# Optimization experiments

Hardware: AMD Instinct MI355X
Metric: run time of the kernel (lower is better)

## Reference

```python
import jax, jax.numpy as jnp
import numpy as np

N = 50000       # num_entities / nodes
E = 100000      # edges
K = 8           # incoming edge-graph neighbors per edge
D_NODE = 64
D_EDGE = 64
H = 4
DH = D_EDGE // H
DIN = D_EDGE + 2 * D_NODE  # [edge_feat, node_feat[src], node_feat[dst]]


def setup_inputs() -> dict:
    key = jax.random.key(0)
    ks = jax.random.split(key, 6)
    node_features = jax.random.normal(ks[0], (N, D_NODE), jnp.float32)
    edge_features = jax.random.normal(ks[1], (E, D_EDGE), jnp.float32)
    edge_index = jax.random.randint(ks[2], (2, E), 0, N)
    node_tiers = jax.random.randint(ks[3], (N,), 0, 4, dtype=jnp.int32)
    # edge adjacency (line graph): each edge attends to K other edges
    adj_dst = jnp.repeat(jnp.arange(E), K)                       # [A]
    adj_src = jax.random.randint(ks[4], (E * K,), 0, E)          # [A]
    # learned params: two EdgeAttention layers, each Wq/Wk/Wv [DIN,D_EDGE], Wo [D_EDGE,D_EDGE]
    wkeys = jax.random.split(ks[5], 8)
    def w(k, fan_in, fan_out):
        return jax.random.normal(k, (fan_in, fan_out), jnp.float32) * np.float32(1.0 / np.sqrt(fan_in))
    params = {}
    for li in (1, 2):
        base = (li - 1) * 4
        params[f'l{li}_Wq'] = w(wkeys[base + 0], DIN, D_EDGE)
        params[f'l{li}_Wk'] = w(wkeys[base + 1], DIN, D_EDGE)
        params[f'l{li}_Wv'] = w(wkeys[base + 2], DIN, D_EDGE)
        params[f'l{li}_Wo'] = w(wkeys[base + 3], D_EDGE, D_EDGE)
    return dict(node_features=node_features, edge_features=edge_features,
                edge_index=edge_index, node_tiers=node_tiers,
                adj_src=adj_src, adj_dst=adj_dst, **params)


def _edge_attention(node_f, edge_f, edge_index, adj_src, adj_dst, Wq, Wk, Wv, Wo):
    # x: edge feature conditioned on endpoint node features  [E, DIN]
    x = jnp.concatenate([edge_f, node_f[edge_index[0]], node_f[edge_index[1]]], axis=-1)
    q = (x @ Wq).reshape(E, H, DH)
    k = (x @ Wk).reshape(E, H, DH)
    v = (x @ Wv).reshape(E, H, DH)
    scale = np.float32(1.0 / np.sqrt(DH))
    # scores per adjacency pair  [A, H]
    s = jnp.einsum('ahd,ahd->ah', q[adj_dst], k[adj_src]) * scale
    # segment softmax over incoming neighbors of each dst edge
    m = jax.ops.segment_max(s, adj_dst, num_segments=E)          # [E, H]
    e = jnp.exp(s - m[adj_dst])                                   # [A, H]
    denom = jax.ops.segment_sum(e, adj_dst, num_segments=E)      # [E, H]
    alpha = e / denom[adj_dst]                                    # [A, H]
    out = jax.ops.segment_sum(alpha[..., None] * v[adj_src], adj_dst, num_segments=E)  # [E,H,DH]
    return edge_f + out.reshape(E, D_EDGE) @ Wo                   # residual


def reference(node_features, edge_features, edge_index, node_tiers, adj_src, adj_dst,
              l1_Wq, l1_Wk, l1_Wv, l1_Wo, l2_Wq, l2_Wk, l2_Wv, l2_Wo):
    ef = _edge_attention(node_features, edge_features, edge_index, adj_src, adj_dst,
                         l1_Wq, l1_Wk, l1_Wv, l1_Wo)
    ef = _edge_attention(node_features, ef, edge_index, adj_src, adj_dst,
                         l2_Wq, l2_Wk, l2_Wv, l2_Wo)
    return ef  # updated edge features of the output DeltaGraph
```

## Files before the change

kernel.cpp:

```cpp
#include <hip/hip_runtime.h>

#define NE 100000
#define NN 50000

typedef short short8 __attribute__((ext_vector_type(8)));
typedef float f32x4 __attribute__((ext_vector_type(4)));
typedef unsigned short ushort;

__device__ inline ushort f2bf(float f) {
    unsigned int u = __float_as_uint(f);
    u += 0x7FFFu + ((u >> 16) & 1u);
    return (ushort)(u >> 16);
}
__device__ inline float bf2f(ushort u) {
    return __uint_as_float((unsigned int)u << 16);
}

__device__ inline short8 pack_bf8(float4 a, float4 b) {
    short8 r;
    r[0] = (short)f2bf(a.x); r[1] = (short)f2bf(a.y);
    r[2] = (short)f2bf(a.z); r[3] = (short)f2bf(a.w);
    r[4] = (short)f2bf(b.x); r[5] = (short)f2bf(b.y);
    r[6] = (short)f2bf(b.z); r[7] = (short)f2bf(b.w);
    return r;
}

__global__ __launch_bounds__(256) void prep_qkv_w(
    const float* __restrict__ Wq, const float* __restrict__ Wk,
    const float* __restrict__ Wv, ushort* __restrict__ wf)
{
    int idx = blockIdx.x * 256 + threadIdx.x;
    if (idx >= 6 * 12 * 64) return;
    int lane = idx & 63;
    int st = idx >> 6;
    int s = st / 12, t = st % 12;
    int n = t * 16 + (lane & 15);
    int kb = s * 32 + (lane >> 4) * 8;
    const float* w = (n < 64) ? Wq : (n < 128) ? Wk : Wv;
    int nn = n & 63;
    #pragma unroll
    for (int j = 0; j < 8; ++j)
        wf[(size_t)idx * 8 + j] = f2bf(w[(size_t)(kb + j) * 64 + nn]);
}

__global__ __launch_bounds__(256) void prep_wo_w(
    const float* __restrict__ Wo, ushort* __restrict__ wf)
{
    int idx = blockIdx.x * 256 + threadIdx.x;
    if (idx >= 2 * 4 * 64) return;
    int lane = idx & 63;
    int st = idx >> 6;
    int s = st / 4, t = st % 4;
    int n = t * 16 + (lane & 15);
    int kb = s * 32 + (lane >> 4) * 8;
    #pragma unroll
    for (int j = 0; j < 8; ++j)
        wf[(size_t)idx * 8 + j] = f2bf(Wo[(size_t)(kb + j) * 64 + n]);
}

__global__ __launch_bounds__(256) void qkv_mfma(
    const float* __restrict__ ef, const float* __restrict__ nodef,
    const int* __restrict__ eidx, const ushort* __restrict__ wfrag,
    ushort* __restrict__ qo, ushort* __restrict__ ko, ushort* __restrict__ vo)
{
    const int wave = threadIdx.x >> 6;
    const int lane = threadIdx.x & 63;
    const int r  = lane & 15;
    const int kg = lane >> 4;
    const int e0 = blockIdx.x * 128 + wave * 32;
    const int eA = e0 + r;
    const int eB = e0 + 16 + r;
    const int eAc = (eA < NE) ? eA : NE - 1;
    const int eBc = (eB < NE) ? eB : NE - 1;

    const float* pA[3] = { ef    + (size_t)eAc * 64,
                           nodef + (size_t)eidx[eAc] * 64,
                           nodef + (size_t)eidx[NE + eAc] * 64 };
    const float* pB[3] = { ef    + (size_t)eBc * 64,
                           nodef + (size_t)eidx[eBc] * 64,
                           nodef + (size_t)eidx[NE + eBc] * 64 };

    const short8* wf = (const short8*)wfrag;
    f32x4 acc0[12], acc1[12];
    #pragma unroll
    for (int t = 0; t < 12; ++t) { acc0[t] = (f32x4)(0.f); acc1[t] = (f32x4)(0.f); }

    #pragma unroll
    for (int s = 0; s < 6; ++s) {
        const float* ba = pA[s >> 1] + (s & 1) * 32 + kg * 8;
        const float* bb = pB[s >> 1] + (s & 1) * 32 + kg * 8;
        short8 a0 = pack_bf8(*(const float4*)ba, *(const float4*)(ba + 4));
        short8 a1 = pack_bf8(*(const float4*)bb, *(const float4*)(bb + 4));
        #pragma unroll
        for (int t = 0; t < 12; ++t) {
            short8 b = wf[(size_t)(s * 12 + t) * 64 + lane];
            acc0[t] = __builtin_amdgcn_mfma_f32_16x16x32_bf16(a0, b, acc0[t], 0, 0, 0);
            acc1[t] = __builtin_amdgcn_mfma_f32_16x16x32_bf16(a1, b, acc1[t], 0, 0, 0);
        }
    }

    const int orow0 = e0 + kg * 4;
    const int orow1 = e0 + 16 + kg * 4;
    #pragma unroll
    for (int t = 0; t < 12; ++t) {
        const int c = t * 16 + r;
        ushort* dst = (c < 64) ? (qo + c) : (c < 128) ? (ko + (c - 64)) : (vo + (c - 128));
        #pragma unroll
        for (int j = 0; j < 4; ++j) {
            int row0 = orow0 + j;
            int row1 = orow1 + j;
            if (row0 < NE) dst[(size_t)row0 * 64] = f2bf(acc0[t][j]);
            if (row1 < NE) dst[(size_t)row1 * 64] = f2bf(acc1[t][j]);
        }
    }
}

__global__ __launch_bounds__(256) void attn_kernel(
    const ushort* __restrict__ q, const ushort* __restrict__ kbuf,
    const ushort* __restrict__ vbuf, const int* __restrict__ adj_src,
    ushort* __restrict__ ao)
{
    const int wid  = (blockIdx.x * 256 + threadIdx.x) >> 6;
    const int lane = threadIdx.x & 63;
    if (wid >= NE) return;
    const int e    = wid;
    const int half = lane >> 5;
    const int l32  = lane & 31;

    ushort2 qu = *(const ushort2*)(q + (size_t)e * 64 + l32 * 2);
    const float q0 = bf2f(qu.x), q1 = bf2f(qu.y);

    int nbr[4];
    float s[4];
    #pragma unroll
    for (int t = 0; t < 4; ++t) {
        nbr[t] = adj_src[e * 8 + 2 * t + half];
        ushort2 ku = *(const ushort2*)(kbuf + (size_t)nbr[t] * 64 + l32 * 2);
        float p = q0 * bf2f(ku.x) + q1 * bf2f(ku.y);
        p += __shfl_xor(p, 1);
        p += __shfl_xor(p, 2);
        p += __shfl_xor(p, 4);
        s[t] = p * 0.25f;
    }

    float m = fmaxf(fmaxf(s[0], s[1]), fmaxf(s[2], s[3]));
    m = fmaxf(m, __shfl_xor(m, 32));
    float w[4], den = 0.f;
    #pragma unroll
    for (int t = 0; t < 4; ++t) { w[t] = __expf(s[t] - m); den += w[t]; }
    den += __shfl_xor(den, 32);
    const float inv = 1.f / den;

    float ox = 0.f, oy = 0.f;
    #pragma unroll
    for (int t = 0; t < 4; ++t) {
        ushort2 vu = *(const ushort2*)(vbuf + (size_t)nbr[t] * 64 + l32 * 2);
        ox = fmaf(w[t], bf2f(vu.x), ox);
        oy = fmaf(w[t], bf2f(vu.y), oy);
    }
    ox = (ox + __shfl_xor(ox, 32)) * inv;
    oy = (oy + __shfl_xor(oy, 32)) * inv;

    if (lane < 32) {
        ushort2 o;
        o.x = f2bf(ox);
        o.y = f2bf(oy);
        *(ushort2*)(ao + (size_t)e * 64 + l32 * 2) = o;
    }
}

__global__ __launch_bounds__(256) void wo_mfma(
    const float* __restrict__ ef_in, const ushort* __restrict__ attn,
    const ushort* __restrict__ wofrag, float* __restrict__ efo)
{
    const int wave = threadIdx.x >> 6;
    const int lane = threadIdx.x & 63;
    const int r  = lane & 15;
    const int kg = lane >> 4;
    const int e0 = blockIdx.x * 64 + wave * 16;
    const int e  = e0 + r;
    const int ec = (e < NE) ? e : NE - 1;

    short8 afr[2];
    #pragma unroll
    for (int s = 0; s < 2; ++s)
        afr[s] = *(const short8*)(attn + (size_t)ec * 64 + s * 32 + kg * 8);

    const short8* wf = (const short8*)wofrag;
    f32x4 acc[4];
    #pragma unroll
    for (int t = 0; t < 4; ++t) acc[t] = (f32x4)(0.f);
    #pragma unroll
    for (int s = 0; s < 2; ++s) {
        #pragma unroll
        for (int t = 0; t < 4; ++t) {
            short8 b = wf[(size_t)(s * 4 + t) * 64 + lane];
            acc[t] = __builtin_amdgcn_mfma_f32_16x16x32_bf16(afr[s], b, acc[t], 0, 0, 0);
        }
    }

    const int orow = e0 + kg * 4;
    #pragma unroll
    for (int t = 0; t < 4; ++t) {
        const int c = t * 16 + r;
        #pragma unroll
        for (int j = 0; j < 4; ++j) {
            int row = orow + j;
            if (row < NE) {
                size_t off = (size_t)row * 64 + c;
                efo[off] = acc[t][j] + ef_in[off];
            }
        }
    }
}

extern "C" void kernel_launch(void* const* d_in, const int* in_sizes, int n_in,
                              void* d_out, int out_size, void* d_ws, size_t ws_size,
                              hipStream_t stream)
{
    const float* nodef   = (const float*)d_in[0];
    const float* ef      = (const float*)d_in[1];
    const int*   eidx    = (const int*)d_in[2];
    const int*   adj_src = (const int*)d_in[4];
    const float* l1Wq = (const float*)d_in[6];
    const float* l1Wk = (const float*)d_in[7];
    const float* l1Wv = (const float*)d_in[8];
    const float* l1Wo = (const float*)d_in[9];
    const float* l2Wq = (const float*)d_in[10];
    const float* l2Wk = (const float*)d_in[11];
    const float* l2Wv = (const float*)d_in[12];
    const float* l2Wo = (const float*)d_in[13];

    ushort* q  = (ushort*)d_ws;
    ushort* k  = q  + (size_t)NE * 64;
    ushort* v  = k  + (size_t)NE * 64;
    ushort* ao = v  + (size_t)NE * 64;
    ushort* wf1 = ao + (size_t)NE * 64;
    ushort* wf2 = wf1 + 36864;
    ushort* wo1 = wf2 + 36864;
    ushort* wo2 = wo1 + 4096;
    float* out = (float*)d_out;

    dim3 blk(256);
    const int gq = (NE + 127) / 128;
    const int ga = (NE + 3) / 4;
    const int gw = (NE + 63) / 64;

    prep_qkv_w<<<18, blk, 0, stream>>>(l1Wq, l1Wk, l1Wv, wf1);
    prep_qkv_w<<<18, blk, 0, stream>>>(l2Wq, l2Wk, l2Wv, wf2);
    prep_wo_w<<<2, blk, 0, stream>>>(l1Wo, wo1);
    prep_wo_w<<<2, blk, 0, stream>>>(l2Wo, wo2);

    qkv_mfma<<<gq, blk, 0, stream>>>(ef, nodef, eidx, wf1, q, k, v);
    attn_kernel<<<ga, blk, 0, stream>>>(q, k, v, adj_src, ao);
    wo_mfma<<<gw, blk, 0, stream>>>(ef, ao, wo1, out);
    qkv_mfma<<<gq, blk, 0, stream>>>(out, nodef, eidx, wf2, q, k, v);
    attn_kernel<<<ga, blk, 0, stream>>>(q, k, v, adj_src, ao);
    wo_mfma<<<gw, blk, 0, stream>>>(out, ao, wo2, out);
}
```

Baseline: 170.0 us.

## Stage QKV weight fragments in LDS via global_load_lds and prefetch A operands

Each block now copies the full packed QKV weight fragment array (72 KB) into shared memory with direct global-to-LDS loads, split across the four waves. The MFMA loop then reads B fragments from LDS instead of global or L2. All six A operands are gathered and packed up front so their loads overlap the weight copy. Launch bounds now ask for two blocks per CU. The large LDS footprint limits occupancy, and every block pays for the 72 KB copy.

```diff
diff --git a/kernel.cpp b/kernel.cpp
--- a/kernel.cpp
+++ b/kernel.cpp
@@ -6,6 +6,7 @@
 typedef short short8 __attribute__((ext_vector_type(8)));
 typedef float f32x4 __attribute__((ext_vector_type(4)));
 typedef unsigned short ushort;
+typedef unsigned int uint;
 
 __device__ inline ushort f2bf(float f) {
     unsigned int u = __float_as_uint(f);
@@ -58,13 +59,29 @@
         wf[(size_t)idx * 8 + j] = f2bf(Wo[(size_t)(kb + j) * 64 + n]);
 }
 
-__global__ __launch_bounds__(256) void qkv_mfma(
+__global__ __launch_bounds__(256, 2) void qkv_mfma(
     const float* __restrict__ ef, const float* __restrict__ nodef,
     const int* __restrict__ eidx, const ushort* __restrict__ wfrag,
     ushort* __restrict__ qo, ushort* __restrict__ ko, ushort* __restrict__ vo)
 {
+    __shared__ __align__(1024) ushort lds_w[36864];
+
     const int wave = threadIdx.x >> 6;
     const int lane = threadIdx.x & 63;
+
+    {
+        const char* g = (const char*)wfrag + (size_t)lane * 16;
+        char*       l = (char*)lds_w;
+        #pragma unroll
+        for (int i = 0; i < 18; ++i) {
+            const int frag = wave * 18 + i;
+            __builtin_amdgcn_global_load_lds(
+                (const __attribute__((address_space(1))) uint*)(g + (size_t)frag * 1024),
+                (__attribute__((address_space(3))) uint*)(l + (size_t)frag * 1024),
+                16, 0, 0);
+        }
+    }
+
     const int r  = lane & 15;
     const int kg = lane >> 4;
     const int e0 = blockIdx.x * 128 + wave * 32;
@@ -80,22 +97,32 @@
                            nodef + (size_t)eidx[eBc] * 64,
                            nodef + (size_t)eidx[NE + eBc] * 64 };
 
-    const short8* wf = (const short8*)wfrag;
-    f32x4 acc0[12], acc1[12];
-    #pragma unroll
-    for (int t = 0; t < 12; ++t) { acc0[t] = (f32x4)(0.f); acc1[t] = (f32x4)(0.f); }
-
+    short8 a0[6], a1[6];
     #pragma unroll
     for (int s = 0; s < 6; ++s) {
         const float* ba = pA[s >> 1] + (s & 1) * 32 + kg * 8;
         const float* bb = pB[s >> 1] + (s & 1) * 32 + kg * 8;
-        short8 a0 = pack_bf8(*(const float4*)ba, *(const float4*)(ba + 4));
-        short8 a1 = pack_bf8(*(const float4*)bb, *(const float4*)(bb + 4));
+        a0[s] = pack_bf8(*(const float4*)ba, *(const float4*)(ba + 4));
+        a1[s] = pack_bf8(*(const float4*)bb, *(const float4*)(bb + 4));
+    }
+
+    f32x4 acc0[12], acc1[12];
+    #pragma unroll
+    for (int t = 0; t < 12; ++t) { acc0[t] = (f32x4)(0.f); acc1[t] = (f32x4)(0.f); }
+
+    __syncthreads();
+
+    const char* lbase = (const char*)lds_w + lane * 16;
+    #pragma unroll
+    for (int s = 0; s < 6; ++s) {
+        short8 b[12];
+        #pragma unroll
+        for (int t = 0; t < 12; ++t)
+            b[t] = *(const short8*)(lbase + (size_t)(s * 12 + t) * 1024);
         #pragma unroll
         for (int t = 0; t < 12; ++t) {
-            short8 b = wf[(size_t)(s * 12 + t) * 64 + lane];
-            acc0[t] = __builtin_amdgcn_mfma_f32_16x16x32_bf16(a0, b, acc0[t], 0, 0, 0);
-            acc1[t] = __builtin_amdgcn_mfma_f32_16x16x32_bf16(a1, b, acc1[t], 0, 0, 0);
+            acc0[t] = __builtin_amdgcn_mfma_f32_16x16x32_bf16(a0[s], b[t], acc0[t], 0, 0, 0);
+            acc1[t] = __builtin_amdgcn_mfma_f32_16x16x32_bf16(a1[s], b[t], acc1[t], 0, 0, 0);
         }
     }
 
```

New measurement: 155.6 us. 8.5% less time.

## Restructure QKV GEMM to stage A tiles in LDS and hold weights in registers

Applied to the files above, without the earlier changes.

The QKV projection kernel now has each block load 64 edge rows (edge features plus gathered src/dst node features) cooperatively with coalesced 64-byte-per-thread reads. It converts them to bf16 and stages them in shared memory. Each wave keeps its 3 output column tiles of weight fragments in registers and loops over four 16-row tiles read from LDS. This replaces the old layout where every wave streamed all 12 weight tiles from global memory and each lane gathered strided A fragments. The cost is a __syncthreads, LDS use, higher register pressure (launch bounds set to 3 blocks), and twice as many blocks, each handling fewer rows.

```diff
diff --git a/kernel.cpp b/kernel.cpp
--- a/kernel.cpp
+++ b/kernel.cpp
@@ -6,6 +6,7 @@
 typedef short short8 __attribute__((ext_vector_type(8)));
 typedef float f32x4 __attribute__((ext_vector_type(4)));
 typedef unsigned short ushort;
+typedef unsigned int uint;
 
 __device__ inline ushort f2bf(float f) {
     unsigned int u = __float_as_uint(f);
@@ -58,59 +59,88 @@
         wf[(size_t)idx * 8 + j] = f2bf(Wo[(size_t)(kb + j) * 64 + n]);
 }
 
-__global__ __launch_bounds__(256) void qkv_mfma(
+__global__ __launch_bounds__(256, 3) void qkv_mfma(
     const float* __restrict__ ef, const float* __restrict__ nodef,
     const int* __restrict__ eidx, const ushort* __restrict__ wfrag,
     ushort* __restrict__ qo, ushort* __restrict__ ko, ushort* __restrict__ vo)
 {
-    const int wave = threadIdx.x >> 6;
-    const int lane = threadIdx.x & 63;
-    const int r  = lane & 15;
-    const int kg = lane >> 4;
-    const int e0 = blockIdx.x * 128 + wave * 32;
-    const int eA = e0 + r;
-    const int eB = e0 + 16 + r;
-    const int eAc = (eA < NE) ? eA : NE - 1;
-    const int eBc = (eB < NE) ? eB : NE - 1;
-
-    const float* pA[3] = { ef    + (size_t)eAc * 64,
-                           nodef + (size_t)eidx[eAc] * 64,
-                           nodef + (size_t)eidx[NE + eAc] * 64 };
-    const float* pB[3] = { ef    + (size_t)eBc * 64,
-                           nodef + (size_t)eidx[eBc] * 64,
-                           nodef + (size_t)eidx[NE + eBc] * 64 };
-
-    const short8* wf = (const short8*)wfrag;
-    f32x4 acc0[12], acc1[12];
-    #pragma unroll
-    for (int t = 0; t < 12; ++t) { acc0[t] = (f32x4)(0.f); acc1[t] = (f32x4)(0.f); }
-
+    __shared__ __align__(16) char lds_a[24 * 1056];
+
+    const int tid = threadIdx.x;
+    const int l   = tid & 63;
+    const int w   = tid >> 6;
+
+    short8 Bf[6][3];
+    #pragma unroll
+    for (int s = 0; s < 6; ++s)
+        #pragma unroll
+        for (int n = 0; n < 3; ++n)
+            Bf[s][n] = *(const short8*)((const char*)wfrag +
+                        (size_t)((s * 12 + 3 * w + n) * 64 + l) * 16);
+
+    {
+        const int r64 = tid >> 2;
+        const int p   = tid & 3;
+        const int row = blockIdx.x * 64 + r64;
+        const int rc  = (row < NE) ? row : NE - 1;
+        const float* srcs[3] = { ef    + (size_t)rc * 64,
+                                 nodef + (size_t)eidx[rc] * 64,
+                                 nodef + (size_t)eidx[NE + rc] * 64 };
+        #pragma unroll
+        for (int c = 0; c < 3; ++c) {
+            const float* sp = srcs[c] + p * 16;
+            float4 f0 = *(const float4*)(sp + 0);
+            float4 f1 = *(const float4*)(sp + 4);
+            float4 f2 = *(const float4*)(sp + 8);
+            float4 f3 = *(const float4*)(sp + 12);
+            short8 lo = pack_bf8(f0, f1);
+            short8 hi = pack_bf8(f2, f3);
+            const int regbase = (w * 3 + c) * 2;
+            *(short8*)(lds_a + (size_t)(regbase + 0) * 1056 + l * 16) = lo;
+            *(short8*)(lds_a + (size_t)(regbase + 1) * 1056 + l * 16) = hi;
+        }
+    }
+
+    f32x4 acc[4][3];
+    #pragma unroll
+    for (int T = 0; T < 4; ++T)
+        #pragma unroll
+        for (int n = 0; n < 3; ++n) acc[T][n] = (f32x4)(0.f);
+
+    __syncthreads();
+
+    const int r  = l & 15;
+    const int kg = l >> 4;
     #pragma unroll
     for (int s = 0; s < 6; ++s) {
-        const float* ba = pA[s >> 1] + (s & 1) * 32 + kg * 8;
-        const float* bb = pB[s >> 1] + (s & 1) * 32 + kg * 8;
-        short8 a0 = pack_bf8(*(const float4*)ba, *(const float4*)(ba + 4));
-        short8 a1 = pack_bf8(*(const float4*)bb, *(const float4*)(bb + 4));
-        #pragma unroll
-        for (int t = 0; t < 12; ++t) {
-            short8 b = wf[(size_t)(s * 12 + t) * 64 + lane];
-            acc0[t] = __builtin_amdgcn_mfma_f32_16x16x32_bf16(a0, b, acc0[t], 0, 0, 0);
-            acc1[t] = __builtin_amdgcn_mfma_f32_16x16x32_bf16(a1, b, acc1[t], 0, 0, 0);
-        }
-    }
-
-    const int orow0 = e0 + kg * 4;
-    const int orow1 = e0 + 16 + kg * 4;
-    #pragma unroll
-    for (int t = 0; t < 12; ++t) {
-        const int c = t * 16 + r;
-        ushort* dst = (c < 64) ? (qo + c) : (c < 128) ? (ko + (c - 64)) : (vo + (c - 128));
-        #pragma unroll
-        for (int j = 0; j < 4; ++j) {
-            int row0 = orow0 + j;
-            int row1 = orow1 + j;
-            if (row0 < NE) dst[(size_t)row0 * 64] = f2bf(acc0[t][j]);
-            if (row1 < NE) dst[(size_t)row1 * 64] = f2bf(acc1[t][j]);
+        short8 Af[4];
+        #pragma unroll
+        for (int T = 0; T < 4; ++T) {
+            const int region = (T * 3 + (s >> 1)) * 2 + (kg & 1);
+            const int slot   = r * 4 + (s & 1) * 2 + (kg >> 1);
+            Af[T] = *(const short8*)(lds_a + (size_t)region * 1056 + slot * 16);
+        }
+        #pragma unroll
+        for (int T = 0; T < 4; ++T)
+            #pragma unroll
+            for (int n = 0; n < 3; ++n)
+                acc[T][n] = __builtin_amdgcn_mfma_f32_16x16x32_bf16(
+                                Af[T], Bf[s][n], acc[T][n], 0, 0, 0);
+    }
+
+    const int e0 = blockIdx.x * 64;
+    #pragma unroll
+    for (int T = 0; T < 4; ++T) {
+        #pragma unroll
+        for (int n = 0; n < 3; ++n) {
+            const int c = (3 * w + n) * 16 + r;
+            ushort* dst = (c < 64) ? (qo + c) : (c < 128) ? (ko + (c - 64))
+                                              : (vo + (c - 128));
+            #pragma unroll
+            for (int jj = 0; jj < 4; ++jj) {
+                const int row = e0 + T * 16 + kg * 4 + jj;
+                if (row < NE) dst[(size_t)row * 64] = f2bf(acc[T][n][jj]);
+            }
         }
     }
 }
@@ -242,7 +272,7 @@
     float* out = (float*)d_out;
 
     dim3 blk(256);
-    const int gq = (NE + 127) / 128;
+    const int gq = (NE + 63) / 64;
     const int ga = (NE + 3) / 4;
     const int gw = (NE + 63) / 64;
 
```

Result: faster. 148.6 us (-12.6%).
